# Kernel optimization log

Hardware: AMD Instinct MI355X
Metric: run time of the kernel (lower is better)

The kernel has to match this reference:

```python
import jax, jax.numpy as jnp
import numpy as np

N, E = 20000, 160000          # nodes, edges
D, ED, H, NH = 32, 16, 64, 4  # node_dim, edge_dim, hidden_dim, num_heads
G, MAXN = 100, 200            # graphs, nodes per graph (equal-size graphs)
HD = H // NH                  # head dim


def setup_inputs() -> dict:
    key = jax.random.key(0)
    ks = jax.random.split(key, 20)
    p = lambda k, shp: jax.random.normal(k, shp, dtype=jnp.float32) * 0.05
    return {
        "x": jax.random.normal(ks[0], (N, D), dtype=jnp.float32),
        "edge_index": jax.random.randint(ks[1], (2, E), 0, N),
        "edge_attr": jax.random.normal(ks[2], (E, ED), dtype=jnp.float32),
        "batch": jnp.arange(N, dtype=jnp.int32) // MAXN,  # 100 graphs x 200 nodes
        "en_w1": p(ks[3], (H, ED)), "en_b1": p(ks[4], (H,)),
        "en_w2": p(ks[5], (D * H, H)), "en_b2": p(ks[6], (D * H,)),
        "root_w": p(ks[7], (D, H)), "conv_b": p(ks[8], (H,)),
        "in_proj_w": p(ks[9], (3 * H, H)), "in_proj_b": p(ks[10], (3 * H,)),
        "out_proj_w": p(ks[11], (H, H)), "out_proj_b": p(ks[12], (H,)),
        "lin1_w": p(ks[13], (H, H)), "lin1_b": p(ks[14], (H,)),
        "lin2_w": p(ks[15], (1, H)), "lin2_b": p(ks[16], (1,)),
    }


def reference(x, edge_index, edge_attr, batch,
              en_w1, en_b1, en_w2, en_b2, root_w, conv_b,
              in_proj_w, in_proj_b, out_proj_w, out_proj_b,
              lin1_w, lin1_b, lin2_w, lin2_b):
    src, dst = edge_index[0], edge_index[1]
    # ---- NNConv: edge MLP -> per-edge weight [E, D, H], gather-matmul-scatter-mean ----
    h = jax.nn.relu(edge_attr @ en_w1.T + en_b1)
    w_e = (h @ en_w2.T + en_b2).reshape(E, D, H)
    msgs = jnp.einsum('ed,edh->eh', x[src], w_e)                 # [E, H]
    agg = jax.ops.segment_sum(msgs, dst, num_segments=N)         # scatter-sum by dest
    cnt = jax.ops.segment_sum(jnp.ones((E,), x.dtype), dst, num_segments=N)
    agg = agg / jnp.maximum(cnt, 1.0)[:, None]                   # mean aggregation
    xh = jax.nn.relu(agg + x @ root_w + conv_b)                  # root weight + bias
    # ---- to_dense_batch (batch is sorted) ----
    counts = jax.ops.segment_sum(jnp.ones((N,), jnp.int32), batch, num_segments=G)
    starts = jnp.concatenate([jnp.zeros((1,), jnp.int32), jnp.cumsum(counts)[:-1]])
    pos = jnp.arange(N, dtype=jnp.int32) - starts[batch]
    dense = jnp.zeros((G, MAXN, H), xh.dtype).at[batch, pos].set(xh)
    mask = jnp.zeros((G, MAXN), bool).at[batch, pos].set(True)
    # ---- MultiheadAttention (self-attn, key_padding_mask = ~mask) ----
    qkv = dense @ in_proj_w.T + in_proj_b                        # [G, MAXN, 3H]
    q, k, v = jnp.split(qkv, 3, axis=-1)
    sh = lambda t: t.reshape(G, MAXN, NH, HD).transpose(0, 2, 1, 3)  # [G, NH, MAXN, HD]
    q, k, v = sh(q), sh(k), sh(v)
    scores = jnp.einsum('gnqd,gnkd->gnqk', q, k) / jnp.sqrt(jnp.float32(HD))
    scores = jnp.where(mask[:, None, None, :], scores, jnp.float32(-1e9))
    attn = jax.nn.softmax(scores, axis=-1)
    ctx = jnp.einsum('gnqk,gnkd->gnqd', attn, v)
    ctx = ctx.transpose(0, 2, 1, 3).reshape(G, MAXN, H)
    attn_out = ctx @ out_proj_w.T + out_proj_b
    # zero out padded positions, masked mean pool
    attn_out = jnp.where(mask[:, :, None], attn_out, 0.0)
    graph_emb = attn_out.sum(axis=1) / mask.sum(axis=1, keepdims=True).astype(attn_out.dtype)
    h1 = jax.nn.relu(graph_emb @ lin1_w.T + lin1_b)
    return (h1 @ lin2_w.T + lin2_b).squeeze(1)                   # [G]
```

## Files before the change

kernel.cpp:

```cpp
#include <hip/hip_runtime.h>
#include <math.h>

#define N_N 20000
#define N_E 160000
#define KA 2112
#define NKB 66

typedef __attribute__((ext_vector_type(8))) short bfrag;
typedef __attribute__((ext_vector_type(4))) float facc;

__device__ __forceinline__ unsigned short f2bf(float f) {
  union { float f; unsigned u; } v; v.f = f;
  unsigned u = v.u;
  return (unsigned short)((u + 0x7FFF + ((u >> 16) & 1)) >> 16);
}
__device__ __forceinline__ unsigned pk2(float a, float b) {
  return (unsigned)f2bf(a) | ((unsigned)f2bf(b) << 16);
}
__device__ __forceinline__ float bflo(unsigned u) {
  union { unsigned u; float f; } v; v.u = u << 16; return v.f;
}
__device__ __forceinline__ float bfhi(unsigned u) {
  union { unsigned u; float f; } v; v.u = u & 0xffff0000u; return v.f;
}

__global__ __launch_bounds__(256) void k_mlp1(const float* __restrict__ ea,
    const float* __restrict__ w1, const float* __restrict__ b1,
    const int* __restrict__ perm, unsigned short* __restrict__ hes) {
  int t = threadIdx.x, w = t >> 6, j = t & 63;
  int e0 = (blockIdx.x * 4 + w) * 8;
  float wr[16];
#pragma unroll
  for (int i = 0; i < 16; ++i) wr[i] = w1[j * 16 + i];
  float bj = b1[j];
#pragma unroll
  for (int q = 0; q < 8; ++q) {
    int e = e0 + q;
    const float* a = ea + (size_t)e * 16;
    float s = bj;
#pragma unroll
    for (int i = 0; i < 16; ++i) s += a[i] * wr[i];
    hes[(size_t)perm[e] * 64 + j] = f2bf(fmaxf(s, 0.f));
  }
}

__global__ __launch_bounds__(256) void k_hist(const int* __restrict__ eidx,
    int* __restrict__ cnt) {
  int e = blockIdx.x * 256 + threadIdx.x;
  atomicAdd(&cnt[eidx[N_E + e]], 1);
}

__global__ __launch_bounds__(1024) void k_scan(int* __restrict__ hist,
    int* __restrict__ starts) {
  __shared__ int part[1024];
  int t = threadIdx.x;
  const int CH = 20;
  int lo = t * CH;
  int hi = lo + CH; if (hi > N_N) hi = N_N;
  int s = 0;
  for (int i = lo; i < hi; ++i) s += hist[i];
  part[t] = s;
  __syncthreads();
  for (int off = 1; off < 1024; off <<= 1) {
    int v = (t >= off) ? part[t - off] : 0;
    __syncthreads();
    part[t] += v;
    __syncthreads();
  }
  int run = (t == 0) ? 0 : part[t - 1];
  for (int i = lo; i < hi; ++i) {
    int h = hist[i];
    starts[i] = run;
    hist[i] = run;
    run += h;
  }
  if (t == 1023) starts[N_N] = part[1023];
}

__global__ __launch_bounds__(256) void k_scatter(const int* __restrict__ eidx,
    int* __restrict__ cur, int* __restrict__ perm, int* __restrict__ srcl) {
  int e = blockIdx.x * 256 + threadIdx.x;
  int dn = eidx[N_E + e];
  int pos = atomicAdd(&cur[dn], 1);
  perm[e] = pos;
  srcl[pos] = eidx[e];
}

__global__ __launch_bounds__(256) void k_pack(const float* __restrict__ w2,
    const float* __restrict__ b2f, const float* __restrict__ rootw,
    const float* __restrict__ inw,
    unsigned short* __restrict__ Bp, unsigned short* __restrict__ B2p) {
  int idx = blockIdx.x * 256 + threadIdx.x;
  if (idx < 135168) {
    int i = idx & 7, l = (idx >> 3) & 63, cbkb = idx >> 9;
    int cb = cbkb & 3, kb = cbkb >> 2;
    int r = kb * 32 + ((l >> 4) << 3) + i;
    int c = (cb << 4) + (l & 15);
    float v;
    if (r < 2048) { int d = r >> 6, k = r & 63; v = w2[((d << 6) + c) * 64 + k]; }
    else if (r < 2080) v = b2f[((r - 2048) << 6) + c];
    else v = rootw[((r - 2080) << 6) + c];
    Bp[idx] = f2bf(v);
  } else if (idx < 135168 + 12288) {
    int k2 = idx - 135168;
    int i = k2 & 7, l = (k2 >> 3) & 63, cbkb = k2 >> 9;
    int cb = cbkb % 12, kb = cbkb / 12;
    int r = kb * 32 + ((l >> 4) << 3) + i;
    int c = (cb << 4) + (l & 15);
    B2p[k2] = f2bf(inw[c * 64 + r]);
  }
}

#define FMA8(hv, base, xv) \
  acc[base + 0] += xv * bflo(hv.x); acc[base + 1] += xv * bfhi(hv.x); \
  acc[base + 2] += xv * bflo(hv.y); acc[base + 3] += xv * bfhi(hv.y); \
  acc[base + 4] += xv * bflo(hv.z); acc[base + 5] += xv * bfhi(hv.z); \
  acc[base + 6] += xv * bflo(hv.w); acc[base + 7] += xv * bfhi(hv.w);

__global__ __launch_bounds__(256) void k_fused(const float* __restrict__ x,
    const unsigned short* __restrict__ hes, const int* __restrict__ starts,
    const int* __restrict__ srcl,
    const unsigned short* __restrict__ Bp, const unsigned short* __restrict__ B2p,
    const float* __restrict__ convb, const float* __restrict__ inb,
    float* __restrict__ Qb, float* __restrict__ Kb, float* __restrict__ Vb) {
  __shared__ unsigned short Ps[16 * KA];
  __shared__ unsigned short xhT[16 * 68];
  int t = threadIdx.x, w = t >> 6, l = t & 63;
  int n0 = blockIdx.x * 16;
  int d0 = l >> 3, hc = (l & 7) * 8;
#pragma unroll 1
  for (int i4 = 0; i4 < 4; ++i4) {
    int m = w * 4 + i4;
    int n = n0 + m;
    int s0 = starts[n], s1 = starts[n + 1];
    float acc[32];
#pragma unroll
    for (int z = 0; z < 32; ++z) acc[z] = 0.f;
    float xs = 0.f;
    int i = s0;
    for (; i + 1 < s1; i += 2) {
      int sr0 = srcl[i], sr1 = srcl[i + 1];
      uint4 h0 = *(const uint4*)(hes + (size_t)i * 64 + hc);
      uint4 h1 = *(const uint4*)(hes + (size_t)(i + 1) * 64 + hc);
      const float* xr0 = x + sr0 * 32;
      const float* xr1 = x + sr1 * 32;
      float a0 = xr0[d0], a1 = xr0[d0 + 8], a2 = xr0[d0 + 16], a3 = xr0[d0 + 24];
      float b0 = xr1[d0], b1 = xr1[d0 + 8], b2 = xr1[d0 + 16], b3 = xr1[d0 + 24];
      FMA8(h0, 0, a0) FMA8(h0, 8, a1) FMA8(h0, 16, a2) FMA8(h0, 24, a3)
      FMA8(h1, 0, b0) FMA8(h1, 8, b1) FMA8(h1, 16, b2) FMA8(h1, 24, b3)
      if (l < 32) xs += xr0[l] + xr1[l];
    }
    if (i < s1) {
      int sr0 = srcl[i];
      uint4 h0 = *(const uint4*)(hes + (size_t)i * 64 + hc);
      const float* xr0 = x + sr0 * 32;
      float a0 = xr0[d0], a1 = xr0[d0 + 8], a2 = xr0[d0 + 16], a3 = xr0[d0 + 24];
      FMA8(h0, 0, a0) FMA8(h0, 8, a1) FMA8(h0, 16, a2) FMA8(h0, 24, a3)
      if (l < 32) xs += xr0[l];
    }
    int s = m & 7;
#pragma unroll
    for (int q = 0; q < 4; ++q) {
      int sc = (l + 64 * q) ^ s;
      uint4 o;
      o.x = pk2(acc[q * 8 + 0], acc[q * 8 + 1]);
      o.y = pk2(acc[q * 8 + 2], acc[q * 8 + 3]);
      o.z = pk2(acc[q * 8 + 4], acc[q * 8 + 5]);
      o.w = pk2(acc[q * 8 + 6], acc[q * 8 + 7]);
      *(uint4*)(Ps + m * KA + sc * 8) = o;
    }
    if (l < 32) {
      int cnt = s1 - s0; if (cnt < 1) cnt = 1;
      int c1 = (256 + (l >> 3)) ^ s, c2 = (260 + (l >> 3)) ^ s;
      Ps[m * KA + c1 * 8 + (l & 7)] = f2bf(xs);
      Ps[m * KA + c2 * 8 + (l & 7)] = f2bf(x[n * 32 + l] * (float)cnt);
    }
  }
  __syncthreads();
  int col = l & 15, sub = l >> 4;
  int sw = col & 7;
  const bfrag* Bb = (const bfrag*)Bp + w * 64 + l;
  facc ac = {0.f, 0.f, 0.f, 0.f};
#pragma unroll 4
  for (int kb = 0; kb < NKB; ++kb) {
    int sc = ((kb << 2) + sub) ^ sw;
    bfrag af = *(const bfrag*)(Ps + col * KA + sc * 8);
    ac = __builtin_amdgcn_mfma_f32_16x16x32_bf16(af, Bb[kb * 256], ac, 0, 0, 0);
  }
  float cv = convb[w * 16 + col];
#pragma unroll
  for (int j = 0; j < 4; ++j) {
    int m = sub * 4 + j, n = n0 + m;
    int cnt = starts[n + 1] - starts[n]; if (cnt < 1) cnt = 1;
    float inv = 1.f / (float)cnt;
    xhT[m * 68 + w * 16 + col] = f2bf(fmaxf(ac[j] * inv + cv, 0.f));
  }
  __syncthreads();
  bfrag af0 = *(const bfrag*)&xhT[col * 68 + sub * 8];
  bfrag af1 = *(const bfrag*)&xhT[col * 68 + 32 + sub * 8];
  const bfrag* B2b = (const bfrag*)B2p + l;
#pragma unroll
  for (int c3 = 0; c3 < 3; ++c3) {
    int cb = w * 3 + c3;
    facc qa = {0.f, 0.f, 0.f, 0.f};
    qa = __builtin_amdgcn_mfma_f32_16x16x32_bf16(af0, B2b[cb * 64], qa, 0, 0, 0);
    qa = __builtin_amdgcn_mfma_f32_16x16x32_bf16(af1, B2b[(12 + cb) * 64], qa, 0, 0, 0);
#pragma unroll
    for (int j = 0; j < 4; ++j) {
      int n = n0 + sub * 4 + j;
      int g = n / 200, p = n - g * 200;
      int c = cb * 16 + col;
      float v = qa[j] + inb[c];
      int part = c >> 6, rem = c & 63, hh = rem >> 4, dd = rem & 15;
      float* dst = (part == 0) ? Qb : (part == 1 ? Kb : Vb);
      dst[(((size_t)g * 4 + hh) * 200 + p) * 16 + dd] = v;
    }
  }
}

__global__ __launch_bounds__(256) void k_attn(const float* __restrict__ Qb,
    const float* __restrict__ Kb, const float* __restrict__ Vb,
    float* __restrict__ ctx) {
  __shared__ unsigned short Ks[224 * 24];
  __shared__ unsigned short Vt[16 * 232];
  __shared__ unsigned short Pl[4][16 * 40];
  int t = threadIdx.x;
  size_t base = (size_t)blockIdx.x * 3200;
  for (int idx = t; idx < 224 * 16; idx += 256) {
    int row = idx >> 4, d = idx & 15;
    float kv = (row < 200) ? Kb[base + idx] : 0.f;
    float vv = (row < 200) ? Vb[base + idx] : 0.f;
    Ks[row * 24 + d] = f2bf(kv);
    Vt[d * 232 + row] = f2bf(vv);
  }
  __syncthreads();
  int w = t >> 6, l = t & 63;
  int sub = l >> 4, col = l & 15;
  for (int qt = w; qt < 13; qt += 4) {
    bfrag qf = {0, 0, 0, 0, 0, 0, 0, 0};
    int q = qt * 16 + col;
    if (sub < 2 && q < 200) {
      const float* qp = Qb + base + q * 16 + sub * 8;
      float4 qa = *(const float4*)qp;
      float4 qb = *(const float4*)(qp + 4);
      qf[0] = (short)f2bf(qa.x); qf[1] = (short)f2bf(qa.y);
      qf[2] = (short)f2bf(qa.z); qf[3] = (short)f2bf(qa.w);
      qf[4] = (short)f2bf(qb.x); qf[5] = (short)f2bf(qb.y);
      qf[6] = (short)f2bf(qb.z); qf[7] = (short)f2bf(qb.w);
    }
    facc o = {0.f, 0.f, 0.f, 0.f};
    float srow0 = 0.f, srow1 = 0.f, srow2 = 0.f, srow3 = 0.f;
    for (int kt2 = 0; kt2 < 7; ++kt2) {
      int kt0 = kt2 * 2, kt1 = kt0 + 1;
      bfrag kf0 = {0, 0, 0, 0, 0, 0, 0, 0};
      bfrag kf1 = {0, 0, 0, 0, 0, 0, 0, 0};
      if (sub < 2) {
        kf0 = *(const bfrag*)&Ks[(kt0 * 16 + col) * 24 + sub * 8];
        kf1 = *(const bfrag*)&Ks[(kt1 * 16 + col) * 24 + sub * 8];
      }
      facc z = {0.f, 0.f, 0.f, 0.f};
      facc s0 = __builtin_amdgcn_mfma_f32_16x16x32_bf16(qf, kf0, z, 0, 0, 0);
      facc s1 = __builtin_amdgcn_mfma_f32_16x16x32_bf16(qf, kf1, z, 0, 0, 0);
      bool ok0 = (kt0 * 16 + col) < 200;
      bool ok1 = (kt1 * 16 + col) < 200;
#pragma unroll
      for (int j = 0; j < 4; ++j) {
        float e0 = ok0 ? __expf(s0[j] * 0.25f) : 0.f;
        float e1 = ok1 ? __expf(s1[j] * 0.25f) : 0.f;
        if (j == 0) { srow0 += e0 + e1; } else if (j == 1) { srow1 += e0 + e1; }
        else if (j == 2) { srow2 += e0 + e1; } else { srow3 += e0 + e1; }
        int qr = (sub << 2) + j;
        Pl[w][qr * 40 + col] = f2bf(e0);
        Pl[w][qr * 40 + 16 + col] = f2bf(e1);
      }
      bfrag pf = *(const bfrag*)&Pl[w][col * 40 + sub * 8];
      bfrag vf = *(const bfrag*)&Vt[col * 232 + kt2 * 32 + sub * 8];
      o = __builtin_amdgcn_mfma_f32_16x16x32_bf16(pf, vf, o, 0, 0, 0);
    }
#pragma unroll
    for (int off = 1; off < 16; off <<= 1) {
      srow0 += __shfl_xor(srow0, off);
      srow1 += __shfl_xor(srow1, off);
      srow2 += __shfl_xor(srow2, off);
      srow3 += __shfl_xor(srow3, off);
    }
#pragma unroll
    for (int j = 0; j < 4; ++j) {
      int qq = qt * 16 + (sub << 2) + j;
      float sr = (j == 0) ? srow0 : (j == 1) ? srow1 : (j == 2) ? srow2 : srow3;
      if (qq < 200) ctx[base + qq * 16 + col] = o[j] / sr;
    }
  }
}

__global__ __launch_bounds__(64) void k_head(const float* __restrict__ ctx,
    const float* __restrict__ ow, const float* __restrict__ ob,
    const float* __restrict__ w1, const float* __restrict__ b1,
    const float* __restrict__ w2, const float* __restrict__ b2,
    float* __restrict__ out) {
  __shared__ float ms[64], es[64];
  int g = blockIdx.x, t = threadIdx.x;
  int hh = t >> 4, dd = t & 15;
  const float* cb = ctx + (((size_t)g * 4 + hh) * 200) * 16 + dd;
  float s = 0.f;
  for (int p = 0; p < 200; ++p) s += cb[p * 16];
  ms[t] = s * (1.f / 200.f);
  __syncthreads();
  float e = ob[t];
  for (int j = 0; j < 64; ++j) e += ow[t * 64 + j] * ms[j];
  es[t] = e;
  __syncthreads();
  float h1 = b1[t];
  for (int j = 0; j < 64; ++j) h1 += w1[t * 64 + j] * es[j];
  h1 = fmaxf(h1, 0.f);
  float pr = h1 * w2[t];
  for (int off = 32; off >= 1; off >>= 1) pr += __shfl_xor(pr, off);
  if (t == 0) out[g] = pr + b2[0];
}

extern "C" void kernel_launch(void* const* d_in, const int* in_sizes, int n_in,
                              void* d_out, int out_size, void* d_ws, size_t ws_size,
                              hipStream_t stream) {
  (void)in_sizes; (void)n_in;
  const float* x      = (const float*)d_in[0];
  const int*   eidx   = (const int*)d_in[1];
  const float* ea     = (const float*)d_in[2];
  const float* en_w1  = (const float*)d_in[4];
  const float* en_b1  = (const float*)d_in[5];
  const float* en_w2  = (const float*)d_in[6];
  const float* en_b2  = (const float*)d_in[7];
  const float* root_w = (const float*)d_in[8];
  const float* conv_b = (const float*)d_in[9];
  const float* in_w   = (const float*)d_in[10];
  const float* in_b   = (const float*)d_in[11];
  const float* out_w  = (const float*)d_in[12];
  const float* out_b  = (const float*)d_in[13];
  const float* l1w    = (const float*)d_in[14];
  const float* l1b    = (const float*)d_in[15];
  const float* l2w    = (const float*)d_in[16];
  const float* l2b    = (const float*)d_in[17];
  float* out = (float*)d_out;

  char* w = (char*)d_ws;
  unsigned short* hes = (unsigned short*)w;
  float* Qb  = (float*)(w + 20480000);
  float* Kb  = (float*)(w + 25600000);
  float* Vb  = (float*)(w + 30720000);
  float* ctx = (float*)(w + 35840000);
  char* r3 = w + 40960000;
  unsigned short* Bp  = (unsigned short*)r3;
  unsigned short* B2p = (unsigned short*)(r3 + 270336);
  int* starts = (int*)(r3 + 270336 + 24576);
  int* perm   = starts + (N_N + 4);
  int* srcl   = perm + N_E;
  int* cursor = srcl + N_E;
  size_t need = 40960000 + 270336 + 24576
              + (size_t)(N_N + 4) * 4 + 2 * (size_t)N_E * 4 + (size_t)N_N * 4;
  if (ws_size < need || out_size < 100) return;

  hipMemsetAsync(cursor, 0, N_N * 4, stream);
  k_pack<<<580, 256, 0, stream>>>(en_w2, en_b2, root_w, in_w, Bp, B2p);
  k_hist<<<N_E / 256, 256, 0, stream>>>(eidx, cursor);
  k_scan<<<1, 1024, 0, stream>>>(cursor, starts);
  k_scatter<<<N_E / 256, 256, 0, stream>>>(eidx, cursor, perm, srcl);
  k_mlp1<<<5000, 256, 0, stream>>>(ea, en_w1, en_b1, perm, hes);
  k_fused<<<1250, 256, 0, stream>>>(x, hes, starts, srcl, Bp, B2p,
                                    conv_b, in_b, Qb, Kb, Vb);
  k_attn<<<400, 256, 0, stream>>>(Qb, Kb, Vb, ctx);
  k_head<<<100, 64, 0, stream>>>(ctx, out_w, out_b, l1w, l1b, l2w, l2b, out);
}
```

Before: 186.9 us.

## Split fused NNConv accumulation into two K-halves to halve LDS and registers

The per-node edge accumulation now runs in two passes over the hidden dimension (32 columns each). Each pass fills a half-size LDS panel and immediately runs its 33 MFMA k-blocks, with the packed weight layout reordered so each half's rows are contiguous. This cuts the shared-memory buffer roughly in half and the accumulator registers from 32 to 16, and the launch bounds now request 4 blocks per CU, all to raise occupancy. A one-edge-ahead software prefetch is added to the gather loop. The cost is that edges, source features and hes are read twice and two extra barriers are added.

```diff
diff --git a/kernel.cpp b/kernel.cpp
--- a/kernel.cpp
+++ b/kernel.cpp
@@ -3,8 +3,7 @@
 
 #define N_N 20000
 #define N_E 160000
-#define KA 2112
-#define NKB 66
+#define PSW 1088
 
 typedef __attribute__((ext_vector_type(8))) short bfrag;
 typedef __attribute__((ext_vector_type(4))) float facc;
@@ -94,8 +93,13 @@
   if (idx < 135168) {
     int i = idx & 7, l = (idx >> 3) & 63, cbkb = idx >> 9;
     int cb = cbkb & 3, kb = cbkb >> 2;
-    int r = kb * 32 + ((l >> 4) << 3) + i;
+    int rr = ((l >> 4) << 3) + i;
     int c = (cb << 4) + (l & 15);
+    int r;
+    if (kb < 32) r = kb * 64 + rr;
+    else if (kb == 32) r = 2048 + rr;
+    else if (kb < 65) r = (kb - 33) * 64 + 32 + rr;
+    else r = 2080 + rr;
     float v;
     if (r < 2048) { int d = r >> 6, k = r & 63; v = w2[((d << 6) + c) * 64 + k]; }
     else if (r < 2080) v = b2f[((r - 2048) << 6) + c];
@@ -117,75 +121,81 @@
   acc[base + 4] += xv * bflo(hv.z); acc[base + 5] += xv * bfhi(hv.z); \
   acc[base + 6] += xv * bflo(hv.w); acc[base + 7] += xv * bfhi(hv.w);
 
-__global__ __launch_bounds__(256) void k_fused(const float* __restrict__ x,
+__global__ __launch_bounds__(256, 4) void k_fused(const float* __restrict__ x,
     const unsigned short* __restrict__ hes, const int* __restrict__ starts,
     const int* __restrict__ srcl,
     const unsigned short* __restrict__ Bp, const unsigned short* __restrict__ B2p,
     const float* __restrict__ convb, const float* __restrict__ inb,
     float* __restrict__ Qb, float* __restrict__ Kb, float* __restrict__ Vb) {
-  __shared__ unsigned short Ps[16 * KA];
+  __shared__ unsigned short Ps[16 * PSW];
   __shared__ unsigned short xhT[16 * 68];
   int t = threadIdx.x, w = t >> 6, l = t & 63;
   int n0 = blockIdx.x * 16;
-  int d0 = l >> 3, hc = (l & 7) * 8;
-#pragma unroll 1
-  for (int i4 = 0; i4 < 4; ++i4) {
-    int m = w * 4 + i4;
-    int n = n0 + m;
-    int s0 = starts[n], s1 = starts[n + 1];
-    float acc[32];
-#pragma unroll
-    for (int z = 0; z < 32; ++z) acc[z] = 0.f;
-    float xs = 0.f;
-    int i = s0;
-    for (; i + 1 < s1; i += 2) {
-      int sr0 = srcl[i], sr1 = srcl[i + 1];
-      uint4 h0 = *(const uint4*)(hes + (size_t)i * 64 + hc);
-      uint4 h1 = *(const uint4*)(hes + (size_t)(i + 1) * 64 + hc);
-      const float* xr0 = x + sr0 * 32;
-      const float* xr1 = x + sr1 * 32;
-      float a0 = xr0[d0], a1 = xr0[d0 + 8], a2 = xr0[d0 + 16], a3 = xr0[d0 + 24];
-      float b0 = xr1[d0], b1 = xr1[d0 + 8], b2 = xr1[d0 + 16], b3 = xr1[d0 + 24];
-      FMA8(h0, 0, a0) FMA8(h0, 8, a1) FMA8(h0, 16, a2) FMA8(h0, 24, a3)
-      FMA8(h1, 0, b0) FMA8(h1, 8, b1) FMA8(h1, 16, b2) FMA8(h1, 24, b3)
-      if (l < 32) xs += xr0[l] + xr1[l];
-    }
-    if (i < s1) {
-      int sr0 = srcl[i];
-      uint4 h0 = *(const uint4*)(hes + (size_t)i * 64 + hc);
-      const float* xr0 = x + sr0 * 32;
-      float a0 = xr0[d0], a1 = xr0[d0 + 8], a2 = xr0[d0 + 16], a3 = xr0[d0 + 24];
-      FMA8(h0, 0, a0) FMA8(h0, 8, a1) FMA8(h0, 16, a2) FMA8(h0, 24, a3)
-      if (l < 32) xs += xr0[l];
-    }
-    int s = m & 7;
-#pragma unroll
-    for (int q = 0; q < 4; ++q) {
-      int sc = (l + 64 * q) ^ s;
-      uint4 o;
-      o.x = pk2(acc[q * 8 + 0], acc[q * 8 + 1]);
-      o.y = pk2(acc[q * 8 + 2], acc[q * 8 + 3]);
-      o.z = pk2(acc[q * 8 + 4], acc[q * 8 + 5]);
-      o.w = pk2(acc[q * 8 + 6], acc[q * 8 + 7]);
-      *(uint4*)(Ps + m * KA + sc * 8) = o;
-    }
-    if (l < 32) {
-      int cnt = s1 - s0; if (cnt < 1) cnt = 1;
-      int c1 = (256 + (l >> 3)) ^ s, c2 = (260 + (l >> 3)) ^ s;
-      Ps[m * KA + c1 * 8 + (l & 7)] = f2bf(xs);
-      Ps[m * KA + c2 * 8 + (l & 7)] = f2bf(x[n * 32 + l] * (float)cnt);
-    }
-  }
-  __syncthreads();
+  int d1 = l >> 2, d2 = d1 + 16, kc = l & 3;
   int col = l & 15, sub = l >> 4;
   int sw = col & 7;
-  const bfrag* Bb = (const bfrag*)Bp + w * 64 + l;
   facc ac = {0.f, 0.f, 0.f, 0.f};
-#pragma unroll 4
-  for (int kb = 0; kb < NKB; ++kb) {
-    int sc = ((kb << 2) + sub) ^ sw;
-    bfrag af = *(const bfrag*)(Ps + col * KA + sc * 8);
-    ac = __builtin_amdgcn_mfma_f32_16x16x32_bf16(af, Bb[kb * 256], ac, 0, 0, 0);
+
+  for (int half = 0; half < 2; ++half) {
+    int hoff = half * 32 + kc * 8;
+#pragma unroll 1
+    for (int i4 = 0; i4 < 4; ++i4) {
+      int m = w * 4 + i4;
+      int n = n0 + m;
+      int s0 = starts[n], s1 = starts[n + 1];
+      float acc[16];
+#pragma unroll
+      for (int z = 0; z < 16; ++z) acc[z] = 0.f;
+      float xs1 = 0.f, xs2 = 0.f;
+      int i = s0;
+      uint4 hp = {0, 0, 0, 0};
+      float xa = 0.f, xb = 0.f;
+      if (i < s1) {
+        int sr = srcl[i];
+        hp = *(const uint4*)(hes + (size_t)i * 64 + hoff);
+        xa = x[sr * 32 + d1]; xb = x[sr * 32 + d2];
+      }
+      while (i < s1) {
+        uint4 h = hp; float va = xa, vb = xb;
+        int inx = i + 1;
+        if (inx < s1) {
+          int sr = srcl[inx];
+          hp = *(const uint4*)(hes + (size_t)inx * 64 + hoff);
+          xa = x[sr * 32 + d1]; xb = x[sr * 32 + d2];
+        }
+        FMA8(h, 0, va) FMA8(h, 8, vb)
+        xs1 += va; xs2 += vb;
+        i = inx;
+      }
+      int s = m & 7;
+      uint4 o0, o1;
+      o0.x = pk2(acc[0], acc[1]);   o0.y = pk2(acc[2], acc[3]);
+      o0.z = pk2(acc[4], acc[5]);   o0.w = pk2(acc[6], acc[7]);
+      o1.x = pk2(acc[8], acc[9]);   o1.y = pk2(acc[10], acc[11]);
+      o1.z = pk2(acc[12], acc[13]); o1.w = pk2(acc[14], acc[15]);
+      *(uint4*)(Ps + m * PSW + (l ^ s) * 8) = o0;
+      *(uint4*)(Ps + m * PSW + ((l + 64) ^ s) * 8) = o1;
+      if (kc == 0) {
+        if (half == 0) {
+          Ps[m * PSW + ((128 + (d1 >> 3)) ^ s) * 8 + (d1 & 7)] = f2bf(xs1);
+          Ps[m * PSW + ((128 + (d2 >> 3)) ^ s) * 8 + (d2 & 7)] = f2bf(xs2);
+        } else {
+          int cnt = s1 - s0; if (cnt < 1) cnt = 1;
+          Ps[m * PSW + ((128 + (d1 >> 3)) ^ s) * 8 + (d1 & 7)] =
+              f2bf(x[n * 32 + d1] * (float)cnt);
+          Ps[m * PSW + ((128 + (d2 >> 3)) ^ s) * 8 + (d2 & 7)] =
+              f2bf(x[n * 32 + d2] * (float)cnt);
+        }
+      }
+    }
+    __syncthreads();
+    const bfrag* Bb = (const bfrag*)Bp + (half * 33) * 256 + w * 64 + l;
+#pragma unroll 3
+    for (int kb = 0; kb < 33; ++kb) {
+      bfrag af = *(const bfrag*)(Ps + col * PSW + (((kb << 2) + sub) ^ sw) * 8);
+      ac = __builtin_amdgcn_mfma_f32_16x16x32_bf16(af, Bb[kb * 256], ac, 0, 0, 0);
+    }
+    __syncthreads();
   }
   float cv = convb[w * 16 + col];
 #pragma unroll
```

Result: slower. 213.0 us (+13.9%).

## Halve per-block work in fused, attention and head kernels for more parallelism

Applied to the files above, without the earlier changes.

The fused NNConv kernel now handles 8 nodes per block instead of 16. This halves LDS use, doubles the grid, and adds an occupancy hint. The MFMA A-rows are duplicated so half of the 16x16 tile is wasted compute. Attention splits each graph-head's query tiles across two blocks, which reloads K/V twice. The head kernel uses 256 threads to parallelise the pooling sum. Together these aim to raise occupancy and wave count on a GPU that was underfilled.

```diff
diff --git a/kernel.cpp b/kernel.cpp
--- a/kernel.cpp
+++ b/kernel.cpp
@@ -117,20 +117,20 @@
   acc[base + 4] += xv * bflo(hv.z); acc[base + 5] += xv * bfhi(hv.z); \
   acc[base + 6] += xv * bflo(hv.w); acc[base + 7] += xv * bfhi(hv.w);
 
-__global__ __launch_bounds__(256) void k_fused(const float* __restrict__ x,
+__global__ __launch_bounds__(256, 4) void k_fused(const float* __restrict__ x,
     const unsigned short* __restrict__ hes, const int* __restrict__ starts,
     const int* __restrict__ srcl,
     const unsigned short* __restrict__ Bp, const unsigned short* __restrict__ B2p,
     const float* __restrict__ convb, const float* __restrict__ inb,
     float* __restrict__ Qb, float* __restrict__ Kb, float* __restrict__ Vb) {
-  __shared__ unsigned short Ps[16 * KA];
-  __shared__ unsigned short xhT[16 * 68];
+  __shared__ unsigned short Ps[8 * KA];
+  __shared__ unsigned short xhT[8 * 68];
   int t = threadIdx.x, w = t >> 6, l = t & 63;
-  int n0 = blockIdx.x * 16;
+  int n0 = blockIdx.x * 8;
   int d0 = l >> 3, hc = (l & 7) * 8;
 #pragma unroll 1
-  for (int i4 = 0; i4 < 4; ++i4) {
-    int m = w * 4 + i4;
+  for (int i4 = 0; i4 < 2; ++i4) {
+    int m = w * 2 + i4;
     int n = n0 + m;
     int s0 = starts[n], s1 = starts[n + 1];
     float acc[32];
@@ -138,6 +138,7 @@
     for (int z = 0; z < 32; ++z) acc[z] = 0.f;
     float xs = 0.f;
     int i = s0;
+#pragma unroll 1
     for (; i + 1 < s1; i += 2) {
       int sr0 = srcl[i], sr1 = srcl[i + 1];
       uint4 h0 = *(const uint4*)(hes + (size_t)i * 64 + hc);
@@ -158,7 +159,7 @@
       FMA8(h0, 0, a0) FMA8(h0, 8, a1) FMA8(h0, 16, a2) FMA8(h0, 24, a3)
       if (l < 32) xs += xr0[l];
     }
-    int s = m & 7;
+    int s = m;
 #pragma unroll
     for (int q = 0; q < 4; ++q) {
       int sc = (l + 64 * q) ^ s;
@@ -178,26 +179,29 @@
   }
   __syncthreads();
   int col = l & 15, sub = l >> 4;
-  int sw = col & 7;
+  int arow = col & 7;
   const bfrag* Bb = (const bfrag*)Bp + w * 64 + l;
   facc ac = {0.f, 0.f, 0.f, 0.f};
 #pragma unroll 4
   for (int kb = 0; kb < NKB; ++kb) {
-    int sc = ((kb << 2) + sub) ^ sw;
-    bfrag af = *(const bfrag*)(Ps + col * KA + sc * 8);
+    int sc = ((kb << 2) + sub) ^ arow;
+    bfrag af = *(const bfrag*)(Ps + arow * KA + sc * 8);
     ac = __builtin_amdgcn_mfma_f32_16x16x32_bf16(af, Bb[kb * 256], ac, 0, 0, 0);
   }
   float cv = convb[w * 16 + col];
 #pragma unroll
   for (int j = 0; j < 4; ++j) {
-    int m = sub * 4 + j, n = n0 + m;
-    int cnt = starts[n + 1] - starts[n]; if (cnt < 1) cnt = 1;
-    float inv = 1.f / (float)cnt;
-    xhT[m * 68 + w * 16 + col] = f2bf(fmaxf(ac[j] * inv + cv, 0.f));
-  }
-  __syncthreads();
-  bfrag af0 = *(const bfrag*)&xhT[col * 68 + sub * 8];
-  bfrag af1 = *(const bfrag*)&xhT[col * 68 + 32 + sub * 8];
+    int m = sub * 4 + j;
+    if (m < 8) {
+      int n = n0 + m;
+      int cnt = starts[n + 1] - starts[n]; if (cnt < 1) cnt = 1;
+      float inv = 1.f / (float)cnt;
+      xhT[m * 68 + w * 16 + col] = f2bf(fmaxf(ac[j] * inv + cv, 0.f));
+    }
+  }
+  __syncthreads();
+  bfrag af0 = *(const bfrag*)&xhT[(col & 7) * 68 + sub * 8];
+  bfrag af1 = *(const bfrag*)&xhT[(col & 7) * 68 + 32 + sub * 8];
   const bfrag* B2b = (const bfrag*)B2p + l;
 #pragma unroll
   for (int c3 = 0; c3 < 3; ++c3) {
@@ -207,13 +211,16 @@
     qa = __builtin_amdgcn_mfma_f32_16x16x32_bf16(af1, B2b[(12 + cb) * 64], qa, 0, 0, 0);
 #pragma unroll
     for (int j = 0; j < 4; ++j) {
-      int n = n0 + sub * 4 + j;
-      int g = n / 200, p = n - g * 200;
-      int c = cb * 16 + col;
-      float v = qa[j] + inb[c];
-      int part = c >> 6, rem = c & 63, hh = rem >> 4, dd = rem & 15;
-      float* dst = (part == 0) ? Qb : (part == 1 ? Kb : Vb);
-      dst[(((size_t)g * 4 + hh) * 200 + p) * 16 + dd] = v;
+      int m = sub * 4 + j;
+      if (m < 8) {
+        int n = n0 + m;
+        int g = n / 200, p = n - g * 200;
+        int c = cb * 16 + col;
+        float v = qa[j] + inb[c];
+        int part = c >> 6, rem = c & 63, hh = rem >> 4, dd = rem & 15;
+        float* dst = (part == 0) ? Qb : (part == 1 ? Kb : Vb);
+        dst[(((size_t)g * 4 + hh) * 200 + p) * 16 + dd] = v;
+      }
     }
   }
 }
@@ -225,7 +232,8 @@
   __shared__ unsigned short Vt[16 * 232];
   __shared__ unsigned short Pl[4][16 * 40];
   int t = threadIdx.x;
-  size_t base = (size_t)blockIdx.x * 3200;
+  int gh = blockIdx.x >> 1, half = blockIdx.x & 1;
+  size_t base = (size_t)gh * 3200;
   for (int idx = t; idx < 224 * 16; idx += 256) {
     int row = idx >> 4, d = idx & 15;
     float kv = (row < 200) ? Kb[base + idx] : 0.f;
@@ -236,7 +244,8 @@
   __syncthreads();
   int w = t >> 6, l = t & 63;
   int sub = l >> 4, col = l & 15;
-  for (int qt = w; qt < 13; qt += 4) {
+  int qlo = half * 7, qhi = half ? 13 : 7;
+  for (int qt = qlo + w; qt < qhi; qt += 4) {
     bfrag qf = {0, 0, 0, 0, 0, 0, 0, 0};
     int q = qt * 16 + col;
     if (sub < 2 && q < 200) {
@@ -293,29 +302,40 @@
   }
 }
 
-__global__ __launch_bounds__(64) void k_head(const float* __restrict__ ctx,
+__global__ __launch_bounds__(256) void k_head(const float* __restrict__ ctx,
     const float* __restrict__ ow, const float* __restrict__ ob,
     const float* __restrict__ w1, const float* __restrict__ b1,
     const float* __restrict__ w2, const float* __restrict__ b2,
     float* __restrict__ out) {
+  __shared__ float pool[4][64];
   __shared__ float ms[64], es[64];
   int g = blockIdx.x, t = threadIdx.x;
-  int hh = t >> 4, dd = t & 15;
+  int q = t >> 6, c = t & 63;
+  int hh = c >> 4, dd = c & 15;
   const float* cb = ctx + (((size_t)g * 4 + hh) * 200) * 16 + dd;
   float s = 0.f;
-  for (int p = 0; p < 200; ++p) s += cb[p * 16];
-  ms[t] = s * (1.f / 200.f);
-  __syncthreads();
-  float e = ob[t];
-  for (int j = 0; j < 64; ++j) e += ow[t * 64 + j] * ms[j];
-  es[t] = e;
-  __syncthreads();
-  float h1 = b1[t];
-  for (int j = 0; j < 64; ++j) h1 += w1[t * 64 + j] * es[j];
-  h1 = fmaxf(h1, 0.f);
-  float pr = h1 * w2[t];
-  for (int off = 32; off >= 1; off >>= 1) pr += __shfl_xor(pr, off);
-  if (t == 0) out[g] = pr + b2[0];
+  for (int p = q; p < 200; p += 4) s += cb[p * 16];
+  pool[q][c] = s;
+  __syncthreads();
+  if (t < 64) {
+    float sm = pool[0][t] + pool[1][t] + pool[2][t] + pool[3][t];
+    ms[t] = sm * (1.f / 200.f);
+  }
+  __syncthreads();
+  if (t < 64) {
+    float e = ob[t];
+    for (int j = 0; j < 64; ++j) e += ow[t * 64 + j] * ms[j];
+    es[t] = e;
+  }
+  __syncthreads();
+  if (t < 64) {
+    float h1 = b1[t];
+    for (int j = 0; j < 64; ++j) h1 += w1[t * 64 + j] * es[j];
+    h1 = fmaxf(h1, 0.f);
+    float pr = h1 * w2[t];
+    for (int off = 32; off >= 1; off >>= 1) pr += __shfl_xor(pr, off);
+    if (t == 0) out[g] = pr + b2[0];
+  }
 }
 
 extern "C" void kernel_launch(void* const* d_in, const int* in_sizes, int n_in,
@@ -364,8 +384,8 @@
   k_scan<<<1, 1024, 0, stream>>>(cursor, starts);
   k_scatter<<<N_E / 256, 256, 0, stream>>>(eidx, cursor, perm, srcl);
   k_mlp1<<<5000, 256, 0, stream>>>(ea, en_w1, en_b1, perm, hes);
-  k_fused<<<1250, 256, 0, stream>>>(x, hes, starts, srcl, Bp, B2p,
+  k_fused<<<2500, 256, 0, stream>>>(x, hes, starts, srcl, Bp, B2p,
                                     conv_b, in_b, Qb, Kb, Vb);
-  k_attn<<<400, 256, 0, stream>>>(Qb, Kb, Vb, ctx);
-  k_head<<<100, 64, 0, stream>>>(ctx, out_w, out_b, l1w, l1b, l2w, l2b, out);
-}
+  k_attn<<<800, 256, 0, stream>>>(Qb, Kb, Vb, ctx);
+  k_head<<<100, 256, 0, stream>>>(ctx, out_w, out_b, l1w, l1b, l2w, l2b, out);
+}
```

Result: no change. 186.9 us (+0.0%).
